# Performance work log

Measured on AMD Instinct MI355X. Metric: run time of the kernel, lower is better.

## Reference

```python
import jax, jax.numpy as jnp
import numpy as np

N_NODES = 100000
N_EDGES = 1600000
F_IN = 512


def setup_inputs() -> dict:
    key = jax.random.key(0)
    ks = jax.random.split(key, 12)
    x = jax.random.normal(ks[0], (N_NODES, F_IN), dtype=jnp.float32)
    edge_index = jax.random.randint(ks[1], (2, N_EDGES), 0, N_NODES, dtype=jnp.int64)
    def glorot(k, fan_in, fan_out):
        lim = np.sqrt(6.0 / (fan_in + fan_out)).astype(np.float32)
        return jax.random.uniform(k, (fan_in, fan_out), jnp.float32, -lim, lim)
    return {
        "x": x,
        "edge_index": edge_index,
        "W1": glorot(ks[2], F_IN, 64), "b1": jnp.zeros((64,), jnp.float32),
        "W2": glorot(ks[3], 64, 32),   "b2": jnp.zeros((32,), jnp.float32),
        "W3": glorot(ks[4], 32, 16),   "b3": jnp.zeros((16,), jnp.float32),
        "Wl": glorot(ks[5], 16, 7),    "bl": jnp.zeros((7,), jnp.float32),
    }


def _gcn_conv(x, W, b, src, dst, norm, n_nodes):
    # GCNConv: h = W^T x, then symmetric-normalized scatter-add aggregation
    h = x @ W                                  # [N, out]
    msg = h[src] * norm[:, None]               # gather + edge-normalize [E', out]
    agg = jax.ops.segment_sum(msg, dst, num_segments=n_nodes)  # scatter-add
    return agg + b


def reference(x, edge_index, W1, b1, W2, b2, W3, b3, Wl, bl):
    n = x.shape[0]
    loop = jnp.arange(n, dtype=edge_index.dtype)
    # add self-loops (PyG GCNConv default)
    src = jnp.concatenate([edge_index[0], loop])
    dst = jnp.concatenate([edge_index[1], loop])
    deg = jax.ops.segment_sum(jnp.ones_like(dst, dtype=x.dtype), dst, num_segments=n)
    dis = jnp.where(deg > 0, jax.lax.rsqrt(deg), 0.0)  # deg^{-1/2}
    norm = dis[src] * dis[dst]                          # [E']

    # dropout is identity in eval mode
    h = jax.nn.relu(_gcn_conv(x, W1, b1, src, dst, norm, n))
    h = jax.nn.relu(_gcn_conv(h, W2, b2, src, dst, norm, n))
    h = _gcn_conv(h, W3, b3, src, dst, norm, n)
    return h @ Wl + bl                                   # [N, 7]
```

## Files before the change

### kernel.cpp

```cpp
#include <hip/hip_runtime.h>


typedef __bf16 bf16x8 __attribute__((ext_vector_type(8)));
typedef short short8v __attribute__((ext_vector_type(8)));
typedef unsigned short ushort8v __attribute__((ext_vector_type(8)));
typedef unsigned short ushort4v __attribute__((ext_vector_type(4)));
typedef float float4v __attribute__((ext_vector_type(4)));

static inline int ceil_div_i(long long a, long long b) { return (int)((a + b - 1) / b); }

#define CAP 16384
#define SCHUNK 8192

__device__ inline unsigned short bf16rne(float f) {
    union { float f; unsigned u; } c; c.f = f;
    unsigned u = c.u;
    u += 0x7fffu + ((u >> 16) & 1u);
    return (unsigned short)(u >> 16);
}
__device__ inline float bf16tof(unsigned short h) {
    return __uint_as_float((unsigned)h << 16);
}

__global__ __launch_bounds__(256) void init_kernel(const float* __restrict__ W1,
                                                   unsigned short* __restrict__ wt,
                                                   int* __restrict__ gtail) {
    const int t = threadIdx.x;
    if (blockIdx.x == 0) gtail[t] = t * CAP;
    for (int i = blockIdx.x * 256 + t; i < 512 * 64; i += gridDim.x * 256) {
        int k = i >> 6, n = i & 63;
        wt[(size_t)n * 512 + k] = bf16rne(W1[i]);
    }
}

__global__ __launch_bounds__(256) void scatter_gemm1_kernel(
        const int* __restrict__ src, const int* __restrict__ dst,
        int* __restrict__ gtail, unsigned* __restrict__ abuf, int E, int EB,
        const float* __restrict__ x, const unsigned short* __restrict__ wt,
        unsigned short* __restrict__ g1, int M) {
    __shared__ int cur[256];
    const int t = threadIdx.x;
    if (blockIdx.x < EB) {
        const int e0 = blockIdx.x * SCHUNK;
        const int e1 = min(e0 + SCHUNK, E);
        cur[t] = 0;
        __syncthreads();
        for (int e = e0 + t; e < e1; e += 256) atomicAdd(&cur[dst[e] >> 9], 1);
        __syncthreads();
        int c = cur[t];
        cur[t] = c ? atomicAdd(&gtail[t], c) : 0;
        __syncthreads();
        for (int e = e0 + t; e < e1; e += 256) {
            int d = dst[e];
            int pos = atomicAdd(&cur[d >> 9], 1);
            abuf[pos] = ((unsigned)(d & 511) << 23) | (unsigned)src[e];
        }
        return;
    }
    const int tile = blockIdx.x - EB;
    const int w = t >> 6, l = t & 63;
    const int lr = l & 15, g = l >> 4;
    const int row = tile * 64 + w * 16 + lr;
    const bool rok = row < M;
    float4v acc[4] = {};
    const float* xp = x + (size_t)row * 512 + g * 8;
    const unsigned short* wp = wt + (size_t)lr * 512 + g * 8;
    #pragma unroll 2
    for (int k0 = 0; k0 < 512; k0 += 32) {
        short8v av;
        if (rok) {
            float4 xa = *(const float4*)(xp + k0);
            float4 xb = *(const float4*)(xp + k0 + 4);
            av[0] = (short)bf16rne(xa.x); av[1] = (short)bf16rne(xa.y);
            av[2] = (short)bf16rne(xa.z); av[3] = (short)bf16rne(xa.w);
            av[4] = (short)bf16rne(xb.x); av[5] = (short)bf16rne(xb.y);
            av[6] = (short)bf16rne(xb.z); av[7] = (short)bf16rne(xb.w);
        } else {
            av = short8v{0, 0, 0, 0, 0, 0, 0, 0};
        }
        bf16x8 a = __builtin_bit_cast(bf16x8, av);
        #pragma unroll
        for (int f = 0; f < 4; ++f) {
            bf16x8 b = *(const bf16x8*)(wp + (size_t)f * 16 * 512 + k0);
            acc[f] = __builtin_amdgcn_mfma_f32_16x16x32_bf16(a, b, acc[f], 0, 0, 0);
        }
    }
    const int ro0 = tile * 64 + w * 16 + 4 * g;
    #pragma unroll
    for (int f = 0; f < 4; ++f)
        #pragma unroll
        for (int r = 0; r < 4; ++r) {
            int ro = ro0 + r;
            if (ro < M) g1[(size_t)ro * 64 + f * 16 + lr] = bf16rne(acc[f][r]);
        }
}

__global__ __launch_bounds__(256) void build_kernel(const int* __restrict__ gtail,
                                                    const unsigned* __restrict__ abuf,
                                                    int* __restrict__ row_start,
                                                    int* __restrict__ row_end,
                                                    float* __restrict__ dis,
                                                    int* __restrict__ csr_src, int M) {
    __shared__ int hist[512];
    __shared__ int cur[512];
    __shared__ int wsum_[4];
    const int b = blockIdx.x, t = threadIdx.x, lane = t & 63, wid = t >> 6;
    const int n0 = b << 9;
    const int s = b * CAP;
    const int e = gtail[b];
    hist[t] = 0; hist[t + 256] = 0;
    __syncthreads();
    for (int i = s + t; i < e; i += 256) atomicAdd(&hist[abuf[i] >> 23], 1);
    __syncthreads();
    int c0 = hist[2 * t], c1 = hist[2 * t + 1];
    int pair = c0 + c1;
    int inc = pair;
    #pragma unroll
    for (int d = 1; d < 64; d <<= 1) {
        int o = __shfl_up(inc, d);
        if (lane >= d) inc += o;
    }
    if (lane == 63) wsum_[wid] = inc;
    __syncthreads();
    int wpre = 0;
    for (int ww = 0; ww < wid; ++ww) wpre += wsum_[ww];
    int excl = wpre + inc - pair;
    int r0 = s + excl, r1 = r0 + c0;
    int n = n0 + 2 * t;
    if (n < M) {
        row_start[n] = r0; row_end[n] = r1;
        dis[n] = rsqrtf((float)(c0 + 1));
    }
    if (n + 1 < M) {
        row_start[n + 1] = r1; row_end[n + 1] = r1 + c1;
        dis[n + 1] = rsqrtf((float)(c1 + 1));
    }
    cur[2 * t] = r0; cur[2 * t + 1] = r1;
    __syncthreads();
    for (int i = s + t; i < e; i += 256) {
        unsigned p = abuf[i];
        int pos = atomicAdd(&cur[p >> 23], 1);
        csr_src[pos] = (int)(p & 0x7fffffu);
    }
}

template <int F, int FOUT, int LPN, bool RELU, bool FINAL, bool EDGEW>
__global__ __launch_bounds__(256) void gather_mlp_kernel(
        const int* __restrict__ row_start, const int* __restrict__ row_end,
        const int* __restrict__ csr_src, const float* __restrict__ dis,
        const unsigned short* __restrict__ gin, const float* __restrict__ bin,
        const float* __restrict__ W, const float* __restrict__ bout,
        void* __restrict__ o_, int M) {
    constexpr int VEC = F / LPN;
    constexpr int NPB = 256 / LPN;
    constexpr int HSS = F + 4;
    __shared__ float Ws[F * FOUT];
    __shared__ float hs[NPB][HSS];
    __shared__ float bs[FINAL ? FOUT : 1];
    const int t = threadIdx.x;
    for (int i = t; i < F * FOUT; i += 256) Ws[i] = W[i];
    if (FINAL && t < FOUT) bs[t] = bout[t];
    const int grp = t / LPN, gl = t % LPN;
    const int n = blockIdx.x * NPB + grp;
    float dn = 0.f;
    if (n < M) {
        const int rs = row_start[n], re = row_end[n];
        dn = dis[n];
        float acc[VEC] = {};
        int i = rs;
        while (i < re) {
            const int take = re - i;
            int s = 0; float wl = 0.f;
            if (gl < take) {
                s = csr_src[i + gl];
                if constexpr (EDGEW) wl = dis[s];
            }
            #pragma unroll
            for (int jj = 0; jj < LPN; ++jj) {
                if (jj < take) {
                    int sj = __shfl(s, jj, LPN);
                    float wj;
                    if constexpr (EDGEW) wj = __shfl(wl, jj, LPN) * dn;
                    if constexpr (VEC == 8) {
                        ushort8v r8 = *(const ushort8v*)(gin + (size_t)sj * F + gl * 8);
                        #pragma unroll
                        for (int k = 0; k < 8; ++k) {
                            float v = bf16tof(r8[k]);
                            if constexpr (EDGEW) acc[k] += wj * v; else acc[k] += v;
                        }
                    } else {
                        ushort4v r4 = *(const ushort4v*)(gin + (size_t)sj * F + gl * 4);
                        #pragma unroll
                        for (int k = 0; k < 4; ++k) {
                            float v = bf16tof(r4[k]);
                            if constexpr (EDGEW) acc[k] += wj * v; else acc[k] += v;
                        }
                    }
                }
            }
            i += LPN;
        }
        const float sw = EDGEW ? dn * dn : 1.f;
        if constexpr (VEC == 8) {
            ushort8v r8 = *(const ushort8v*)(gin + (size_t)n * F + gl * 8);
            #pragma unroll
            for (int k = 0; k < 8; ++k) acc[k] += sw * bf16tof(r8[k]);
        } else {
            ushort4v r4 = *(const ushort4v*)(gin + (size_t)n * F + gl * 4);
            #pragma unroll
            for (int k = 0; k < 4; ++k) acc[k] += sw * bf16tof(r4[k]);
        }
        #pragma unroll
        for (int k = 0; k < VEC; ++k) {
            float pre = EDGEW ? acc[k] : dn * acc[k];
            float r = pre + bin[gl * VEC + k];
            if (RELU) r = fmaxf(r, 0.f);
            hs[grp][gl * VEC + k] = r;
        }
    }
    __syncthreads();
    if (!FINAL) {
        constexpr int OCPT = FOUT / LPN;
        if (n < M) {
            const int oc0 = gl * OCPT;
            float a[OCPT] = {};
            #pragma unroll
            for (int k = 0; k < F; ++k) {
                float hv = hs[grp][k];
                if constexpr (OCPT == 4) {
                    float4 wv = *(const float4*)&Ws[k * FOUT + oc0];
                    a[0] += hv * wv.x; a[1] += hv * wv.y;
                    a[2] += hv * wv.z; a[3] += hv * wv.w;
                } else {
                    float2 wv = *(const float2*)&Ws[k * FOUT + oc0];
                    a[0] += hv * wv.x; a[1] += hv * wv.y;
                }
            }
            unsigned short* o = (unsigned short*)o_;
            if constexpr (OCPT == 4) {
                ushort4v pk;
                #pragma unroll
                for (int j = 0; j < 4; ++j) pk[j] = bf16rne(a[j] * dn);
                *(ushort4v*)(o + (size_t)n * FOUT + oc0) = pk;
            } else {
                #pragma unroll
                for (int j = 0; j < OCPT; ++j)
                    o[(size_t)n * FOUT + oc0 + j] = bf16rne(a[j] * dn);
            }
        }
    } else {
        float* o = (float*)o_;
        for (int idx = t; idx < NPB * FOUT; idx += 256) {
            int nl = idx / FOUT, oc = idx % FOUT;
            int nn = blockIdx.x * NPB + nl;
            if (nn >= M) continue;
            float a = bs[oc];
            #pragma unroll
            for (int k = 0; k < F; ++k) a += hs[nl][k] * Ws[k * FOUT + oc];
            o[(size_t)nn * FOUT + oc] = a;
        }
    }
}

extern "C" void kernel_launch(void* const* d_in, const int* in_sizes, int n_in,
                              void* d_out, int out_size, void* d_ws, size_t ws_size,
                              hipStream_t stream) {
    const float* x  = (const float*)d_in[0];
    const int* eidx = (const int*)d_in[1];
    const float* W1 = (const float*)d_in[2];
    const float* b1 = (const float*)d_in[3];
    const float* W2 = (const float*)d_in[4];
    const float* b2 = (const float*)d_in[5];
    const float* W3 = (const float*)d_in[6];
    const float* b3 = (const float*)d_in[7];
    const float* Wl = (const float*)d_in[8];
    const float* bl = (const float*)d_in[9];
    float* out = (float*)d_out;

    const int M = in_sizes[0] / 512;
    const int E = in_sizes[1] / 2;
    const int* src = eidx;
    const int* dst = eidx + E;
    const int NB = ceil_div_i(M, 512);
    const int EB = ceil_div_i(E, SCHUNK);
    const int NT = ceil_div_i(M, 64);

    char* ws = (char*)d_ws;
    const size_t szM1 = ((size_t)(M + 1) * 4 + 255) & ~(size_t)255;
    const size_t szAR = ((size_t)NB * CAP * 4 + 255) & ~(size_t)255;
    size_t off = 0;
    int*      gtail     = (int*)(ws + off); off += 1024;
    int*      row_start = (int*)(ws + off); off += szM1;
    int*      row_end   = (int*)(ws + off); off += szM1;
    float*    dis       = (float*)(ws + off); off += szM1;
    unsigned* abuf      = (unsigned*)(ws + off); off += szAR;
    int*      csr_src   = (int*)(ws + off); off += szAR;
    unsigned short* wt  = (unsigned short*)(ws + off); off += 66560;
    unsigned short* g1  = (unsigned short*)(ws + off);
    off += ((size_t)M * 64 * 2 + 255) & ~(size_t)255;
    unsigned short* g2  = (unsigned short*)(ws + off);
    off += ((size_t)M * 32 * 2 + 255) & ~(size_t)255;
    unsigned short* g3  = (unsigned short*)(ws + off);
    off += ((size_t)M * 16 * 2 + 255) & ~(size_t)255;

    init_kernel<<<128, 256, 0, stream>>>(W1, wt, gtail);
    scatter_gemm1_kernel<<<EB + NT, 256, 0, stream>>>(src, dst, gtail, abuf, E, EB,
                                                      x, wt, g1, M);
    build_kernel<<<NB, 256, 0, stream>>>(gtail, abuf, row_start, row_end, dis, csr_src, M);

    gather_mlp_kernel<64, 32, 8, true, false, true><<<ceil_div_i(M, 32), 256, 0, stream>>>(
        row_start, row_end, csr_src, dis, g1, b1, W2, nullptr, g2, M);
    gather_mlp_kernel<32, 16, 8, true, false, false><<<ceil_div_i(M, 32), 256, 0, stream>>>(
        row_start, row_end, csr_src, dis, g2, b2, W3, nullptr, g3, M);
    gather_mlp_kernel<16, 7, 4, false, true, false><<<ceil_div_i(M, 64), 256, 0, stream>>>(
        row_start, row_end, csr_src, dis, g3, b3, Wl, bl, out, M);
}
```

Baseline: 214.4 us.

## Stage X tiles in LDS via direct global-to-LDS loads and enlarge GEMM1 tile

Result: faster. 180.4 us (median of 3 runs) (-15.8%).

```diff
diff --git a/kernel.cpp b/kernel.cpp
--- a/kernel.cpp
+++ b/kernel.cpp
@@ -11,6 +11,12 @@
 
 #define CAP 16384
 #define SCHUNK 8192
+#define RPB 128
+
+#define GLOAD_LDS16(gsrc, ldst)                                                  \
+    __builtin_amdgcn_global_load_lds(                                            \
+        (const __attribute__((address_space(1))) unsigned*)(gsrc),               \
+        (__attribute__((address_space(3))) unsigned*)(ldst), 16, 0, 0)
 
 __device__ inline unsigned short bf16rne(float f) {
     union { float f; unsigned u; } c; c.f = f;
@@ -39,6 +45,8 @@
         const float* __restrict__ x, const unsigned short* __restrict__ wt,
         unsigned short* __restrict__ g1, int M) {
     __shared__ int cur[256];
+    __shared__ __align__(16) char xs[RPB * 32 * 4];
+    __shared__ __align__(16) unsigned short wst[64 * 40];
     const int t = threadIdx.x;
     if (blockIdx.x < EB) {
         const int e0 = blockIdx.x * SCHUNK;
@@ -60,39 +68,68 @@
     const int tile = blockIdx.x - EB;
     const int w = t >> 6, l = t & 63;
     const int lr = l & 15, g = l >> 4;
-    const int row = tile * 64 + w * 16 + lr;
-    const bool rok = row < M;
-    float4v acc[4] = {};
-    const float* xp = x + (size_t)row * 512 + g * 8;
-    const unsigned short* wp = wt + (size_t)lr * 512 + g * 8;
-    #pragma unroll 2
-    for (int k0 = 0; k0 < 512; k0 += 32) {
-        short8v av;
-        if (rok) {
-            float4 xa = *(const float4*)(xp + k0);
-            float4 xb = *(const float4*)(xp + k0 + 4);
+    const int row0 = tile * RPB;
+    float4v acc[2][4] = {};
+
+    for (int c = 0; c < 16; ++c) {
+        const int k0 = c * 32;
+        if (c) __syncthreads();
+        {
+            char* ldsb = xs + w * 4096;
+            #pragma unroll
+            for (int j = 0; j < 4; ++j) {
+                int o = w * 4096 + j * 1024 + l * 16;
+                int r = o >> 7;
+                int colb = (o & 127) ^ ((r & 7) << 4);
+                int grow = row0 + r;
+                if (grow >= M) grow = 0;
+                const char* gs = (const char*)x + (size_t)grow * 2048 +
+                                 (size_t)k0 * 4 + colb;
+                GLOAD_LDS16(gs, ldsb + j * 1024);
+            }
+        }
+        {
+            int n = t >> 2, q = t & 3;
+            ushort8v v = *(const ushort8v*)(wt + (size_t)n * 512 + k0 + q * 8);
+            *(ushort8v*)&wst[n * 40 + q * 8] = v;
+        }
+        __syncthreads();
+        bf16x8 bf[4];
+        #pragma unroll
+        for (int f = 0; f < 4; ++f)
+            bf[f] = *(const bf16x8*)&wst[(f * 16 + lr) * 40 + g * 8];
+        #pragma unroll
+        for (int st = 0; st < 2; ++st) {
+            const int r = w * 32 + st * 16 + lr;
+            const int swz = (r & 7) << 4;
+            const char* base = xs + r * 128;
+            float4 xa = *(const float4*)(base + ((g * 32) ^ swz));
+            float4 xb = *(const float4*)(base + ((g * 32 + 16) ^ swz));
+            short8v av;
             av[0] = (short)bf16rne(xa.x); av[1] = (short)bf16rne(xa.y);
             av[2] = (short)bf16rne(xa.z); av[3] = (short)bf16rne(xa.w);
             av[4] = (short)bf16rne(xb.x); av[5] = (short)bf16rne(xb.y);
             av[6] = (short)bf16rne(xb.z); av[7] = (short)bf16rne(xb.w);
-        } else {
-            av = short8v{0, 0, 0, 0, 0, 0, 0, 0};
-        }
-        bf16x8 a = __builtin_bit_cast(bf16x8, av);
-        #pragma unroll
-        for (int f = 0; f < 4; ++f) {
-            bf16x8 b = *(const bf16x8*)(wp + (size_t)f * 16 * 512 + k0);
-            acc[f] = __builtin_amdgcn_mfma_f32_16x16x32_bf16(a, b, acc[f], 0, 0, 0);
-        }
-    }
-    const int ro0 = tile * 64 + w * 16 + 4 * g;
+            bf16x8 a = __builtin_bit_cast(bf16x8, av);
+            #pragma unroll
+            for (int f = 0; f < 4; ++f)
+                acc[st][f] = __builtin_amdgcn_mfma_f32_16x16x32_bf16(a, bf[f],
+                                                                     acc[st][f], 0, 0, 0);
+        }
+    }
     #pragma unroll
-    for (int f = 0; f < 4; ++f)
+    for (int st = 0; st < 2; ++st) {
+        const int ro0 = row0 + w * 32 + st * 16 + 4 * g;
         #pragma unroll
         for (int r = 0; r < 4; ++r) {
             int ro = ro0 + r;
-            if (ro < M) g1[(size_t)ro * 64 + f * 16 + lr] = bf16rne(acc[f][r]);
-        }
+            if (ro < M) {
+                #pragma unroll
+                for (int f = 0; f < 4; ++f)
+                    g1[(size_t)ro * 64 + f * 16 + lr] = bf16rne(acc[st][f][r]);
+            }
+        }
+    }
 }
 
 __global__ __launch_bounds__(256) void build_kernel(const int* __restrict__ gtail,
@@ -283,7 +320,7 @@
     const int* dst = eidx + E;
     const int NB = ceil_div_i(M, 512);
     const int EB = ceil_div_i(E, SCHUNK);
-    const int NT = ceil_div_i(M, 64);
+    const int NT = ceil_div_i(M, RPB);
 
     char* ws = (char*)d_ws;
     const size_t szM1 = ((size_t)(M + 1) * 4 + 255) & ~(size_t)255;
```

## Interleave scatter and GEMM blocks and software-pipeline x loads in GEMM1

Applied to the files above, without the earlier changes.

Result: no change. 212.2 us (-1.0%).

```diff
diff --git a/kernel.cpp b/kernel.cpp
--- a/kernel.cpp
+++ b/kernel.cpp
@@ -33,6 +33,35 @@
     }
 }
 
+#define GLOADX(XV, BASE)                                                     \
+    {                                                                        \
+        _Pragma("unroll")                                                    \
+        for (int j = 0; j < 4; ++j) {                                        \
+            XV[2 * j]     = *(const float4*)(xp + (BASE) + j * 32);          \
+            XV[2 * j + 1] = *(const float4*)(xp + (BASE) + j * 32 + 4);      \
+        }                                                                    \
+    }
+#define GCOMP(XV, BASE)                                                      \
+    {                                                                        \
+        _Pragma("unroll")                                                    \
+        for (int j = 0; j < 4; ++j) {                                        \
+            const int k0 = (BASE) + j * 32;                                  \
+            float4 xa_ = XV[2 * j], xb_ = XV[2 * j + 1];                     \
+            short8v av;                                                      \
+            av[0] = (short)bf16rne(xa_.x); av[1] = (short)bf16rne(xa_.y);    \
+            av[2] = (short)bf16rne(xa_.z); av[3] = (short)bf16rne(xa_.w);    \
+            av[4] = (short)bf16rne(xb_.x); av[5] = (short)bf16rne(xb_.y);    \
+            av[6] = (short)bf16rne(xb_.z); av[7] = (short)bf16rne(xb_.w);    \
+            bf16x8 a = __builtin_bit_cast(bf16x8, av);                       \
+            _Pragma("unroll")                                                \
+            for (int f = 0; f < 4; ++f) {                                    \
+                bf16x8 b = *(const bf16x8*)(wp + f * 8192 + k0);             \
+                acc[f] = __builtin_amdgcn_mfma_f32_16x16x32_bf16(a, b,       \
+                                                                 acc[f], 0, 0, 0); \
+            }                                                                \
+        }                                                                    \
+    }
+
 __global__ __launch_bounds__(256) void scatter_gemm1_kernel(
         const int* __restrict__ src, const int* __restrict__ dst,
         int* __restrict__ gtail, unsigned* __restrict__ abuf, int E, int EB,
@@ -40,52 +69,46 @@
         unsigned short* __restrict__ g1, int M) {
     __shared__ int cur[256];
     const int t = threadIdx.x;
-    if (blockIdx.x < EB) {
-        const int e0 = blockIdx.x * SCHUNK;
-        const int e1 = min(e0 + SCHUNK, E);
-        cur[t] = 0;
-        __syncthreads();
-        for (int e = e0 + t; e < e1; e += 256) atomicAdd(&cur[dst[e] >> 9], 1);
-        __syncthreads();
-        int c = cur[t];
-        cur[t] = c ? atomicAdd(&gtail[t], c) : 0;
-        __syncthreads();
-        for (int e = e0 + t; e < e1; e += 256) {
-            int d = dst[e];
-            int pos = atomicAdd(&cur[d >> 9], 1);
-            abuf[pos] = ((unsigned)(d & 511) << 23) | (unsigned)src[e];
-        }
-        return;
-    }
-    const int tile = blockIdx.x - EB;
+    int gt;
+    if (blockIdx.x < 2 * EB) {
+        if (!(blockIdx.x & 1)) {
+            const int e0 = (blockIdx.x >> 1) * SCHUNK;
+            const int e1 = min(e0 + SCHUNK, E);
+            cur[t] = 0;
+            __syncthreads();
+            for (int e = e0 + t; e < e1; e += 256) atomicAdd(&cur[dst[e] >> 9], 1);
+            __syncthreads();
+            int c = cur[t];
+            cur[t] = c ? atomicAdd(&gtail[t], c) : 0;
+            __syncthreads();
+            for (int e = e0 + t; e < e1; e += 256) {
+                int d = dst[e];
+                int pos = atomicAdd(&cur[d >> 9], 1);
+                abuf[pos] = ((unsigned)(d & 511) << 23) | (unsigned)src[e];
+            }
+            return;
+        }
+        gt = blockIdx.x >> 1;
+    } else {
+        gt = blockIdx.x - EB;
+    }
     const int w = t >> 6, l = t & 63;
     const int lr = l & 15, g = l >> 4;
-    const int row = tile * 64 + w * 16 + lr;
-    const bool rok = row < M;
+    const int row = gt * 64 + w * 16 + lr;
+    const int rowc = (row < M) ? row : 0;
+    const float* xp = x + (size_t)rowc * 512 + g * 8;
+    const unsigned short* wp = wt + (size_t)lr * 512 + g * 8;
     float4v acc[4] = {};
-    const float* xp = x + (size_t)row * 512 + g * 8;
-    const unsigned short* wp = wt + (size_t)lr * 512 + g * 8;
-    #pragma unroll 2
-    for (int k0 = 0; k0 < 512; k0 += 32) {
-        short8v av;
-        if (rok) {
-            float4 xa = *(const float4*)(xp + k0);
-            float4 xb = *(const float4*)(xp + k0 + 4);
-            av[0] = (short)bf16rne(xa.x); av[1] = (short)bf16rne(xa.y);
-            av[2] = (short)bf16rne(xa.z); av[3] = (short)bf16rne(xa.w);
-            av[4] = (short)bf16rne(xb.x); av[5] = (short)bf16rne(xb.y);
-            av[6] = (short)bf16rne(xb.z); av[7] = (short)bf16rne(xb.w);
-        } else {
-            av = short8v{0, 0, 0, 0, 0, 0, 0, 0};
-        }
-        bf16x8 a = __builtin_bit_cast(bf16x8, av);
-        #pragma unroll
-        for (int f = 0; f < 4; ++f) {
-            bf16x8 b = *(const bf16x8*)(wp + (size_t)f * 16 * 512 + k0);
-            acc[f] = __builtin_amdgcn_mfma_f32_16x16x32_bf16(a, b, acc[f], 0, 0, 0);
-        }
-    }
-    const int ro0 = tile * 64 + w * 16 + 4 * g;
+    float4 xa[8], xb[8];
+    GLOADX(xa, 0);
+    GLOADX(xb, 128);
+    GCOMP(xa, 0);
+    GLOADX(xa, 256);
+    GCOMP(xb, 128);
+    GLOADX(xb, 384);
+    GCOMP(xa, 256);
+    GCOMP(xb, 384);
+    const int ro0 = gt * 64 + w * 16 + 4 * g;
     #pragma unroll
     for (int f = 0; f < 4; ++f)
         #pragma unroll
```

## Stage X tile into swizzled LDS as bf16 before MFMA in GEMM1

Applied to the files above, without the earlier changes.

After: 205.9 us. -4.0%, faster.

```diff
diff --git a/kernel.cpp b/kernel.cpp
--- a/kernel.cpp
+++ b/kernel.cpp
@@ -38,9 +38,10 @@
         int* __restrict__ gtail, unsigned* __restrict__ abuf, int E, int EB,
         const float* __restrict__ x, const unsigned short* __restrict__ wt,
         unsigned short* __restrict__ g1, int M) {
-    __shared__ int cur[256];
+    __shared__ __align__(16) char smem[64 * 512 * 2];
     const int t = threadIdx.x;
     if (blockIdx.x < EB) {
+        int* cur = (int*)smem;
         const int e0 = blockIdx.x * SCHUNK;
         const int e1 = min(e0 + SCHUNK, E);
         cur[t] = 0;
@@ -58,34 +59,49 @@
         return;
     }
     const int tile = blockIdx.x - EB;
+    const int row0 = tile * 64;
+    const float* tb = x + (size_t)row0 * 512;
+
+    #pragma unroll
+    for (int o = 0; o < 4; ++o) {
+        float4 v[8];
+        #pragma unroll
+        for (int j = 0; j < 8; ++j) {
+            int e = ((o * 8 + j) * 256 + t) * 4;
+            int r = e >> 9;
+            int ge = (row0 + r < M) ? e : (e & 511);
+            v[j] = *(const float4*)(tb + ge);
+        }
+        #pragma unroll
+        for (int j = 0; j < 8; ++j) {
+            int e = ((o * 8 + j) * 256 + t) * 4;
+            int r = e >> 9, k = e & 511;
+            int byte = r * 1024 + ((k * 2) ^ ((r & 7) << 4));
+            ushort4v pk;
+            pk[0] = bf16rne(v[j].x); pk[1] = bf16rne(v[j].y);
+            pk[2] = bf16rne(v[j].z); pk[3] = bf16rne(v[j].w);
+            *(ushort4v*)(smem + byte) = pk;
+        }
+    }
+    __syncthreads();
+
     const int w = t >> 6, l = t & 63;
     const int lr = l & 15, g = l >> 4;
-    const int row = tile * 64 + w * 16 + lr;
-    const bool rok = row < M;
+    const int lrow = w * 16 + lr;
+    const int rbase = lrow * 1024;
+    const int rswz = (lrow & 7) << 4;
+    const unsigned short* wp = wt + (size_t)lr * 512 + g * 8;
     float4v acc[4] = {};
-    const float* xp = x + (size_t)row * 512 + g * 8;
-    const unsigned short* wp = wt + (size_t)lr * 512 + g * 8;
-    #pragma unroll 2
-    for (int k0 = 0; k0 < 512; k0 += 32) {
-        short8v av;
-        if (rok) {
-            float4 xa = *(const float4*)(xp + k0);
-            float4 xb = *(const float4*)(xp + k0 + 4);
-            av[0] = (short)bf16rne(xa.x); av[1] = (short)bf16rne(xa.y);
-            av[2] = (short)bf16rne(xa.z); av[3] = (short)bf16rne(xa.w);
-            av[4] = (short)bf16rne(xb.x); av[5] = (short)bf16rne(xb.y);
-            av[6] = (short)bf16rne(xb.z); av[7] = (short)bf16rne(xb.w);
-        } else {
-            av = short8v{0, 0, 0, 0, 0, 0, 0, 0};
-        }
-        bf16x8 a = __builtin_bit_cast(bf16x8, av);
+    #pragma unroll 4
+    for (int c = 0; c < 16; ++c) {
+        bf16x8 a = *(const bf16x8*)(smem + rbase + ((c * 64 + g * 16) ^ rswz));
         #pragma unroll
         for (int f = 0; f < 4; ++f) {
-            bf16x8 b = *(const bf16x8*)(wp + (size_t)f * 16 * 512 + k0);
+            bf16x8 b = *(const bf16x8*)(wp + f * 8192 + c * 32);
             acc[f] = __builtin_amdgcn_mfma_f32_16x16x32_bf16(a, b, acc[f], 0, 0, 0);
         }
     }
-    const int ro0 = tile * 64 + w * 16 + 4 * g;
+    const int ro0 = row0 + w * 16 + 4 * g;
     #pragma unroll
     for (int f = 0; f < 4; ++f)
         #pragma unroll
```
